# Optimization experiments

Hardware: AMD Instinct MI355X
Metric: run time of the kernel (lower is better)

Reference implementation:

```python
import jax, jax.numpy as jnp
import numpy as np
from math import sqrt

H = 16
D_MODEL = 1024
D_K = D_MODEL // H
B, S = 2, 2048


def setup_inputs() -> dict:
    key = jax.random.key(0)
    ks = jax.random.split(key, 12)
    scale = 1.0 / sqrt(D_MODEL)
    inp = {
        "query": jax.random.normal(ks[0], (B, S, D_MODEL), jnp.float32),
        "key": jax.random.normal(ks[1], (B, S, D_MODEL), jnp.float32),
        "value": jax.random.normal(ks[2], (B, S, D_MODEL), jnp.float32),
        # causal mask [B, S, S]; module unsqueezes head dim itself
        "mask": jnp.broadcast_to(jnp.tril(jnp.ones((S, S), jnp.int32)), (B, S, S)),
        "Wq": jax.random.normal(ks[3], (D_MODEL, D_MODEL), jnp.float32) * scale,
        "bq": jnp.zeros((D_MODEL,), jnp.float32),
        "Wk": jax.random.normal(ks[4], (D_MODEL, D_MODEL), jnp.float32) * scale,
        "bk": jnp.zeros((D_MODEL,), jnp.float32),
        "Wv": jax.random.normal(ks[5], (D_MODEL, D_MODEL), jnp.float32) * scale,
        "bv": jnp.zeros((D_MODEL,), jnp.float32),
        "Wo": jax.random.normal(ks[6], (D_MODEL, D_MODEL), jnp.float32) * scale,
        "bo": jnp.zeros((D_MODEL,), jnp.float32),
    }
    return inp


def reference(query, key, value, mask, Wq, bq, Wk, bk, Wv, bv, Wo, bo):
    nb = query.shape[0]

    def proj(x, W, b):
        # nn.Linear: x @ W.T + b, then split heads -> [B, H, S, D_K]
        y = jnp.einsum('bsd,ed->bse', x, W) + b
        return y.reshape(nb, -1, H, D_K).transpose(0, 2, 1, 3)

    q = proj(query, Wq, bq)
    k = proj(key, Wk, bk)
    v = proj(value, Wv, bv)

    scores = jnp.einsum('bhqd,bhkd->bhqk', q, k) / sqrt(D_K)  # [B,H,S,S]
    scores = jnp.where(mask[:, None, :, :] == 0, -jnp.inf, scores)
    probs = jax.nn.softmax(scores, axis=-1)  # dropout in eval mode (identity)
    ctx = jnp.einsum('bhqk,bhkd->bhqd', probs, v)
    ctx = ctx.transpose(0, 2, 1, 3).reshape(nb, -1, H * D_K)
    return jnp.einsum('bsd,ed->bse', ctx, Wo) + bo
```

## Files before the change

kernel.cpp:

```cpp
#include <hip/hip_runtime.h>
#include <hip/hip_bf16.h>
#include <stdint.h>


#define H_ 16
#define DM 1024
#define DK_ 64
#define BB 2
#define SS 2048
#define PSTR 72

typedef __bf16 bf16x8 __attribute__((ext_vector_type(8)));
typedef __bf16 bf16x2_t __attribute__((ext_vector_type(2)));
typedef float f32x4 __attribute__((ext_vector_type(4)));

#define GLOAD_LDS16(g, l)                                            \
  __builtin_amdgcn_global_load_lds(                                  \
      (__attribute__((address_space(1))) void*)(g),                  \
      (__attribute__((address_space(3))) void*)(l), 16, 0, 0)

__device__ __forceinline__ unsigned short f2bf_u(float f) {
  unsigned int u = __float_as_uint(f);
  u += 0x7fffu + ((u >> 16) & 1u);
  return (unsigned short)(u >> 16);
}

__device__ __forceinline__ unsigned int pack_bf16(float a, float b) {
#if __has_builtin(__builtin_amdgcn_cvt_pk_bf16_f32)
  bf16x2_t v = __builtin_amdgcn_cvt_pk_bf16_f32(a, b);
  unsigned int u;
  __builtin_memcpy(&u, &v, 4);
  return u;
#else
  return (unsigned int)f2bf_u(a) | ((unsigned int)f2bf_u(b) << 16);
#endif
}

__device__ __forceinline__ float fexp2(float x) {
#if __has_builtin(__builtin_amdgcn_exp2f)
  return __builtin_amdgcn_exp2f(x);
#else
  return exp2f(x);
#endif
}

struct Cvt {
  const float* s[7];
  unsigned short* d[7];
  int n[7];
};

__global__ __launch_bounds__(256) void convert_kernel(Cvt c) {
  const int y = blockIdx.y;
  const float* __restrict__ src = c.s[y];
  unsigned short* __restrict__ dst = c.d[y];
  const int nv = c.n[y] >> 2;
  for (int i = blockIdx.x * 256 + threadIdx.x; i < nv; i += 1024 * 256) {
    float4 v = *(const float4*)(src + (size_t)i * 4);
    ushort4 o;
    o.x = f2bf_u(v.x); o.y = f2bf_u(v.y); o.z = f2bf_u(v.z); o.w = f2bf_u(v.w);
    *(ushort4*)(dst + (size_t)i * 4) = o;
  }
}

template <int DUMMY = 0>
__device__ __forceinline__ void gemm_core(
    const unsigned short* __restrict__ A, const unsigned short* __restrict__ W,
    unsigned short* As, unsigned short* Bs, int m0, int n0, int k0, int k1,
    f32x4 (*acc)[4]) {
  const int tid = threadIdx.x;
  const int wave = tid >> 6, lane = tid & 63;
  const int lm = lane & 15, quad = lane >> 4;
  const int wm = (wave >> 1) * 64, wn = (wave & 1) * 64;
  const int srow = lane >> 2;
  const int scol = (lane & 3) * 8;

#pragma unroll
  for (int i = 0; i < 4; ++i)
#pragma unroll
    for (int j = 0; j < 4; ++j) {
      f32x4 z = {0.f, 0.f, 0.f, 0.f};
      acc[i][j] = z;
    }

  for (int kt = k0; kt < k1; kt += 32) {
#pragma unroll
    for (int cc = 0; cc < 2; ++cc) {
      int c = wave * 2 + cc;
      GLOAD_LDS16(A + (size_t)(m0 + c * 16 + srow) * DM + kt + scol,
                  As + c * 512 + lane * 8);
      GLOAD_LDS16(W + (size_t)(n0 + c * 16 + srow) * DM + kt + scol,
                  Bs + c * 512 + lane * 8);
    }
    __syncthreads();
    bf16x8 af[4], bfr[4];
#pragma unroll
    for (int i = 0; i < 4; ++i)
      af[i] = *(const bf16x8*)(As + (wm + i * 16 + lm) * 32 + quad * 8);
#pragma unroll
    for (int j = 0; j < 4; ++j)
      bfr[j] = *(const bf16x8*)(Bs + (wn + j * 16 + lm) * 32 + quad * 8);
#pragma unroll
    for (int i = 0; i < 4; ++i)
#pragma unroll
      for (int j = 0; j < 4; ++j)
        acc[i][j] = __builtin_amdgcn_mfma_f32_16x16x32_bf16(af[i], bfr[j],
                                                            acc[i][j], 0, 0, 0);
    __syncthreads();
  }
}

__global__ __launch_bounds__(256) void qkv_gemm(
    const unsigned short* Qi, const unsigned short* Ki, const unsigned short* Vi,
    const unsigned short* Wq, const unsigned short* Wk, const unsigned short* Wv,
    const float* bq, const float* bk, const float* bv,
    unsigned short* Qf, unsigned short* Kf, unsigned short* Vf) {
  __shared__ unsigned short As[128 * 32], Bs[128 * 32];
  const int z = blockIdx.z;
  const unsigned short* A = z == 0 ? Qi : (z == 1 ? Ki : Vi);
  const unsigned short* W = z == 0 ? Wq : (z == 1 ? Wk : Wv);
  const float* bias = z == 0 ? bq : (z == 1 ? bk : bv);
  const float scale = z == 0 ? 0.125f : 1.0f;
  const int m0 = blockIdx.y * 128, n0 = blockIdx.x * 128;
  f32x4 acc[4][4];
  gemm_core(A, W, As, Bs, m0, n0, 0, DM, acc);
  const int lane = threadIdx.x & 63, wave = threadIdx.x >> 6;
  const int lm = lane & 15, quad = lane >> 4;
  const int wm = (wave >> 1) * 64, wn = (wave & 1) * 64;
  if (z == 2) {
#pragma unroll
    for (int j = 0; j < 4; ++j) {
      int gn = n0 + wn + j * 16 + lm;
      float bv_ = bias[gn];
      int h2 = gn >> 6, dk = gn & 63;
      int a = dk >> 4, ln = dk & 15;
#pragma unroll
      for (int i = 0; i < 4; ++i) {
        int s0 = m0 + wm + i * 16 + quad * 4;
        int b2 = s0 >> 11, sl = s0 & 2047;
        int kt2 = sl >> 6, cc = (sl >> 5) & 1, qk = (sl >> 3) & 3, j0 = sl & 7;
        size_t base =
            ((size_t)(((b2 * 16 + h2) * 32 + kt2) * 4 + a) * 2 + cc) * 512 +
            (qk * 16 + ln) * 8 + j0;
        uint2 w;
        w.x = pack_bf16(acc[i][j][0] + bv_, acc[i][j][1] + bv_);
        w.y = pack_bf16(acc[i][j][2] + bv_, acc[i][j][3] + bv_);
        *(uint2*)(Vf + base) = w;
      }
    }
  } else {
    unsigned short* out = z == 0 ? Qf : Kf;
#pragma unroll
    for (int j = 0; j < 4; ++j) {
      int gn = n0 + wn + j * 16 + lm;
      float bv_ = bias[gn];
      int h2 = gn >> 6, d64 = gn & 63;
      int cc = (d64 >> 5) & 1, qk = (d64 >> 3) & 3, jj = d64 & 7;
#pragma unroll
      for (int i = 0; i < 4; ++i)
#pragma unroll
        for (int r = 0; r < 4; ++r) {
          int gm = m0 + wm + i * 16 + quad * 4 + r;
          int b2 = gm >> 11, sl = gm & 2047;
          size_t base =
              ((size_t)((b2 * 16 + h2) * 128 + (sl >> 4)) * 2 + cc) * 512 +
              (qk * 16 + (sl & 15)) * 8 + jj;
          out[base] = f2bf_u((acc[i][j][r] + bv_) * scale);
        }
    }
  }
}

__global__ __launch_bounds__(256) void o_gemm_sk(
    const unsigned short* Ctx, const unsigned short* Wo,
    float* P0, float* P1) {
  __shared__ unsigned short As[128 * 32], Bs[128 * 32];
  const int m0 = blockIdx.y * 128, n0 = blockIdx.x * 128, ks = blockIdx.z;
  f32x4 acc[4][4];
  gemm_core(Ctx, Wo, As, Bs, m0, n0, ks * 512, ks * 512 + 512, acc);
  const int lane = threadIdx.x & 63, wave = threadIdx.x >> 6;
  const int lm = lane & 15, quad = lane >> 4;
  const int wm = (wave >> 1) * 64, wn = (wave & 1) * 64;
  float* dst = ks ? P1 : P0;
#pragma unroll
  for (int j = 0; j < 4; ++j) {
    int gn = n0 + wn + j * 16 + lm;
#pragma unroll
    for (int i = 0; i < 4; ++i)
#pragma unroll
      for (int r = 0; r < 4; ++r) {
        int gm = m0 + wm + i * 16 + quad * 4 + r;
        dst[(size_t)gm * DM + gn] = acc[i][j][r];
      }
  }
}

__global__ __launch_bounds__(256) void o_reduce(
    const float4* __restrict__ P0, const float4* __restrict__ P1,
    const float* __restrict__ bo, float4* __restrict__ out) {
  for (int i = blockIdx.x * 256 + threadIdx.x; i < 1048576; i += 1024 * 256) {
    float4 a = P0[i], b = P1[i];
    float4 bb = *(const float4*)(bo + (i & 255) * 4);
    float4 o;
    o.x = a.x + b.x + bb.x; o.y = a.y + b.y + bb.y;
    o.z = a.z + b.z + bb.z; o.w = a.w + b.w + bb.w;
    out[i] = o;
  }
}

__global__ __launch_bounds__(256, 4) void attn_kernel(
    const unsigned short* __restrict__ Qf, const unsigned short* __restrict__ Kf,
    const unsigned short* __restrict__ Vf, unsigned short* __restrict__ Ctx) {
  __shared__ unsigned short Ps[4][16 * PSTR];
  const int p = blockIdx.x;
  const int bh = p & 31, qb0 = p >> 5;
  const int qb = (bh & 1) ? (31 - qb0) : qb0;
  const int b = bh >> 4, h = bh & 15;
  const int tid = threadIdx.x, wave = tid >> 6, lane = tid & 63;
  const int lm = lane & 15, quad = lane >> 4;
  const float L2E = 1.4426950408889634f;

  const int qbase = qb * 64 + wave * 16;
  const int nkw = qb + 1;

  bf16x8 qf[2];
#pragma unroll
  for (int c = 0; c < 2; ++c)
    qf[c] = *(const bf16x8*)(Qf +
        ((size_t)(bh * 128 + (qbase >> 4)) * 2 + c) * 512 + lane * 8);

  const unsigned short* Kb = Kf + (size_t)bh * 256 * 512;
  const unsigned short* Vb = Vf + (size_t)bh * 256 * 512;
  unsigned short* Pw = Ps[wave];

  float lsum = 0.f;
  f32x4 oacc[4];
#pragma unroll
  for (int a = 0; a < 4; ++a) {
    f32x4 z = {0.f, 0.f, 0.f, 0.f};
    oacc[a] = z;
  }

  for (int kt = 0; kt < nkw; ++kt) {
    bf16x8 kf[4][2];
#pragma unroll
    for (int ik = 0; ik < 4; ++ik)
#pragma unroll
      for (int c = 0; c < 2; ++c)
        kf[ik][c] = *(const bf16x8*)(Kb +
            ((size_t)(kt * 4 + ik) * 2 + c) * 512 + lane * 8);
    f32x4 s[4];
#pragma unroll
    for (int ik = 0; ik < 4; ++ik) {
      f32x4 z = {0.f, 0.f, 0.f, 0.f};
      z = __builtin_amdgcn_mfma_f32_16x16x32_bf16(kf[ik][0], qf[0], z, 0, 0, 0);
      s[ik] = __builtin_amdgcn_mfma_f32_16x16x32_bf16(kf[ik][1], qf[1], z, 0, 0, 0);
    }
    if (kt == nkw - 1) {
#pragma unroll
      for (int ik = 0; ik < 4; ++ik)
#pragma unroll
        for (int r = 0; r < 4; ++r) {
          int kg = kt * 64 + ik * 16 + quad * 4 + r;
          int qg = qbase + lm;
          if (kg > qg) s[ik][r] = -1e30f;
        }
    }

    bf16x8 vf[4][2];
#pragma unroll
    for (int a = 0; a < 4; ++a)
#pragma unroll
      for (int c = 0; c < 2; ++c)
        vf[a][c] = *(const bf16x8*)(Vb +
            ((size_t)(kt * 8 + a * 2 + c)) * 512 + lane * 8);

#pragma unroll
    for (int ik = 0; ik < 4; ++ik) {
      float p0 = fexp2(s[ik][0] * L2E);
      float p1 = fexp2(s[ik][1] * L2E);
      float p2 = fexp2(s[ik][2] * L2E);
      float p3 = fexp2(s[ik][3] * L2E);
      lsum += (p0 + p1) + (p2 + p3);
      uint2 w;
      w.x = pack_bf16(p0, p1);
      w.y = pack_bf16(p2, p3);
      *(uint2*)(Pw + lm * PSTR + ik * 16 + quad * 4) = w;
    }

    bf16x8 pf[2];
#pragma unroll
    for (int c = 0; c < 2; ++c)
      pf[c] = *(const bf16x8*)(Pw + lm * PSTR + c * 32 + quad * 8);
#pragma unroll
    for (int a = 0; a < 4; ++a) {
      oacc[a] = __builtin_amdgcn_mfma_f32_16x16x32_bf16(pf[0], vf[a][0], oacc[a], 0, 0, 0);
      oacc[a] = __builtin_amdgcn_mfma_f32_16x16x32_bf16(pf[1], vf[a][1], oacc[a], 0, 0, 0);
    }
  }

  lsum += __shfl_xor(lsum, 16);
  lsum += __shfl_xor(lsum, 32);
#pragma unroll
  for (int r = 0; r < 4; ++r) {
    float inv = 1.0f / __shfl(lsum, quad * 4 + r);
    int qg = qbase + quad * 4 + r;
#pragma unroll
    for (int a = 0; a < 4; ++a)
      Ctx[(size_t)(b * SS + qg) * DM + h * DK_ + a * 16 + lm] =
          f2bf_u(oacc[a][r] * inv);
  }
}

extern "C" void kernel_launch(void* const* d_in, const int* in_sizes, int n_in,
                              void* d_out, int out_size, void* d_ws, size_t ws_size,
                              hipStream_t stream) {
  const float* q = (const float*)d_in[0];
  const float* k = (const float*)d_in[1];
  const float* v = (const float*)d_in[2];
  const float* Wq = (const float*)d_in[4];
  const float* bq = (const float*)d_in[5];
  const float* Wk = (const float*)d_in[6];
  const float* bk = (const float*)d_in[7];
  const float* Wv = (const float*)d_in[8];
  const float* bv = (const float*)d_in[9];
  const float* Wo = (const float*)d_in[10];
  const float* bo = (const float*)d_in[11];

  const size_t NX = (size_t)BB * SS * DM;
  const size_t NW = (size_t)DM * DM;
  unsigned short* ws = (unsigned short*)d_ws;
  unsigned short* Qi = ws;
  unsigned short* Ki = Qi + NX;
  unsigned short* Vi = Ki + NX;
  unsigned short* Wqb = Vi + NX;
  unsigned short* Wkb = Wqb + NW;
  unsigned short* Wvb = Wkb + NW;
  unsigned short* Wob = Wvb + NW;
  unsigned short* Qfr = Wob + NW;
  unsigned short* Kfr = Qfr + NX;
  unsigned short* Vfr = Kfr + NX;
  unsigned short* Ctx = Vfr + NX;
  float* P0 = (float*)ws;
  float* P1 = (float*)Qfr;

  Cvt c;
  c.s[0] = q; c.s[1] = k; c.s[2] = v; c.s[3] = Wq; c.s[4] = Wk; c.s[5] = Wv; c.s[6] = Wo;
  c.d[0] = Qi; c.d[1] = Ki; c.d[2] = Vi; c.d[3] = Wqb; c.d[4] = Wkb; c.d[5] = Wvb; c.d[6] = Wob;
  c.n[0] = c.n[1] = c.n[2] = (int)NX;
  c.n[3] = c.n[4] = c.n[5] = c.n[6] = (int)NW;

  dim3 blk(256);
  convert_kernel<<<dim3(1024, 7), blk, 0, stream>>>(c);
  qkv_gemm<<<dim3(8, 32, 3), blk, 0, stream>>>(Qi, Ki, Vi, Wqb, Wkb, Wvb,
                                               bq, bk, bv, Qfr, Kfr, Vfr);
  attn_kernel<<<dim3(1024), blk, 0, stream>>>(Qfr, Kfr, Vfr, Ctx);
  o_gemm_sk<<<dim3(8, 32, 2), blk, 0, stream>>>(Ctx, Wob, P0, P1);
  o_reduce<<<dim3(1024), blk, 0, stream>>>((const float4*)P0, (const float4*)P1,
                                           bo, (float4*)d_out);
}
```

Before: 263.3 us.

## Fuse fp32-to-bf16 activation conversion into QKV GEMM A-tile loads and swizzle block order

Stops converting the query, key and value activations to bf16 in a separate pass. The QKV GEMM now reads fp32 activations directly, packs them to bf16 in registers and stores them to LDS, so only the weights still go through the conversion kernel. This removes a full write and re-read of three activation tensors. The QKV and output-projection GEMMs also move to a 1D grid with a remapped block order that groups M tiles per chunk, likely for L2 reuse. The cost is that A loads in the QKV GEMM become synchronous register loads instead of async global-to-LDS copies, and they fetch twice the bytes per element.

Result: slower. 292.4 us (+11.1%).

```diff
diff --git a/kernel.cpp b/kernel.cpp
--- a/kernel.cpp
+++ b/kernel.cpp
@@ -45,17 +45,15 @@
 }
 
 struct Cvt {
-  const float* s[7];
-  unsigned short* d[7];
-  int n[7];
+  const float* s[4];
+  unsigned short* d[4];
 };
 
 __global__ __launch_bounds__(256) void convert_kernel(Cvt c) {
   const int y = blockIdx.y;
   const float* __restrict__ src = c.s[y];
   unsigned short* __restrict__ dst = c.d[y];
-  const int nv = c.n[y] >> 2;
-  for (int i = blockIdx.x * 256 + threadIdx.x; i < nv; i += 1024 * 256) {
+  for (int i = blockIdx.x * 256 + threadIdx.x; i < (1 << 18); i += 256 * 256) {
     float4 v = *(const float4*)(src + (size_t)i * 4);
     ushort4 o;
     o.x = f2bf_u(v.x); o.y = f2bf_u(v.y); o.z = f2bf_u(v.z); o.w = f2bf_u(v.w);
@@ -110,20 +108,80 @@
   }
 }
 
+template <int DUMMY = 0>
+__device__ __forceinline__ void gemm_core_f32A(
+    const float* __restrict__ A, const unsigned short* __restrict__ W,
+    unsigned short* As, unsigned short* Bs, int m0, int n0,
+    f32x4 (*acc)[4]) {
+  const int tid = threadIdx.x;
+  const int wave = tid >> 6, lane = tid & 63;
+  const int lm = lane & 15, quad = lane >> 4;
+  const int wm = (wave >> 1) * 64, wn = (wave & 1) * 64;
+  const int srow = lane >> 2;
+  const int scol = (lane & 3) * 8;
+  const int arow = tid >> 1, acol = (tid & 1) * 16;
+
+#pragma unroll
+  for (int i = 0; i < 4; ++i)
+#pragma unroll
+    for (int j = 0; j < 4; ++j) {
+      f32x4 z = {0.f, 0.f, 0.f, 0.f};
+      acc[i][j] = z;
+    }
+
+  for (int kt = 0; kt < DM; kt += 32) {
+#pragma unroll
+    for (int cc = 0; cc < 2; ++cc) {
+      int c = wave * 2 + cc;
+      GLOAD_LDS16(W + (size_t)(n0 + c * 16 + srow) * DM + kt + scol,
+                  Bs + c * 512 + lane * 8);
+    }
+    const float* ga = A + (size_t)(m0 + arow) * DM + kt + acol;
+    float4 f0 = *(const float4*)(ga);
+    float4 f1 = *(const float4*)(ga + 4);
+    float4 f2 = *(const float4*)(ga + 8);
+    float4 f3 = *(const float4*)(ga + 12);
+    uint4 u0 = {pack_bf16(f0.x, f0.y), pack_bf16(f0.z, f0.w),
+                pack_bf16(f1.x, f1.y), pack_bf16(f1.z, f1.w)};
+    uint4 u1 = {pack_bf16(f2.x, f2.y), pack_bf16(f2.z, f2.w),
+                pack_bf16(f3.x, f3.y), pack_bf16(f3.z, f3.w)};
+    *(uint4*)(As + arow * 32 + acol) = u0;
+    *(uint4*)(As + arow * 32 + acol + 8) = u1;
+    __syncthreads();
+    bf16x8 af[4], bfr[4];
+#pragma unroll
+    for (int i = 0; i < 4; ++i)
+      af[i] = *(const bf16x8*)(As + (wm + i * 16 + lm) * 32 + quad * 8);
+#pragma unroll
+    for (int j = 0; j < 4; ++j)
+      bfr[j] = *(const bf16x8*)(Bs + (wn + j * 16 + lm) * 32 + quad * 8);
+#pragma unroll
+    for (int i = 0; i < 4; ++i)
+#pragma unroll
+      for (int j = 0; j < 4; ++j)
+        acc[i][j] = __builtin_amdgcn_mfma_f32_16x16x32_bf16(af[i], bfr[j],
+                                                            acc[i][j], 0, 0, 0);
+    __syncthreads();
+  }
+}
+
 __global__ __launch_bounds__(256) void qkv_gemm(
-    const unsigned short* Qi, const unsigned short* Ki, const unsigned short* Vi,
+    const float* q32, const float* k32, const float* v32,
     const unsigned short* Wq, const unsigned short* Wk, const unsigned short* Wv,
     const float* bq, const float* bk, const float* bv,
     unsigned short* Qf, unsigned short* Kf, unsigned short* Vf) {
   __shared__ unsigned short As[128 * 32], Bs[128 * 32];
-  const int z = blockIdx.z;
-  const unsigned short* A = z == 0 ? Qi : (z == 1 ? Ki : Vi);
+  const int p = blockIdx.x;
+  const int c = p & 7, jj0 = p >> 3;
+  const int x = jj0 & 7, yy = (jj0 >> 3) & 3, z = jj0 >> 5;
+  const int y = c * 4 + yy;
+  const int m0 = y * 128, n0 = x * 128;
+  const float* A = z == 0 ? q32 : (z == 1 ? k32 : v32);
   const unsigned short* W = z == 0 ? Wq : (z == 1 ? Wk : Wv);
   const float* bias = z == 0 ? bq : (z == 1 ? bk : bv);
   const float scale = z == 0 ? 0.125f : 1.0f;
-  const int m0 = blockIdx.y * 128, n0 = blockIdx.x * 128;
   f32x4 acc[4][4];
-  gemm_core(A, W, As, Bs, m0, n0, 0, DM, acc);
+  gemm_core_f32A(A, W, As, Bs, m0, n0, acc);
   const int lane = threadIdx.x & 63, wave = threadIdx.x >> 6;
   const int lm = lane & 15, quad = lane >> 4;
   const int wm = (wave >> 1) * 64, wn = (wave & 1) * 64;
@@ -155,7 +213,7 @@
       int gn = n0 + wn + j * 16 + lm;
       float bv_ = bias[gn];
       int h2 = gn >> 6, d64 = gn & 63;
-      int cc = (d64 >> 5) & 1, qk = (d64 >> 3) & 3, jj = d64 & 7;
+      int cc = (d64 >> 5) & 1, qk = (d64 >> 3) & 3, jjq = d64 & 7;
 #pragma unroll
       for (int i = 0; i < 4; ++i)
 #pragma unroll
@@ -164,7 +222,7 @@
           int b2 = gm >> 11, sl = gm & 2047;
           size_t base =
               ((size_t)((b2 * 16 + h2) * 128 + (sl >> 4)) * 2 + cc) * 512 +
-              (qk * 16 + (sl & 15)) * 8 + jj;
+              (qk * 16 + (sl & 15)) * 8 + jjq;
           out[base] = f2bf_u((acc[i][j][r] + bv_) * scale);
         }
     }
@@ -175,7 +233,11 @@
     const unsigned short* Ctx, const unsigned short* Wo,
     float* P0, float* P1) {
   __shared__ unsigned short As[128 * 32], Bs[128 * 32];
-  const int m0 = blockIdx.y * 128, n0 = blockIdx.x * 128, ks = blockIdx.z;
+  const int p = blockIdx.x;
+  const int c = p & 7, jj0 = p >> 3;
+  const int x = jj0 & 7, yy = (jj0 >> 3) & 3, ks = jj0 >> 5;
+  const int y = c * 4 + yy;
+  const int m0 = y * 128, n0 = x * 128;
   f32x4 acc[4][4];
   gemm_core(Ctx, Wo, As, Bs, m0, n0, ks * 512, ks * 512 + 512, acc);
   const int lane = threadIdx.x & 63, wave = threadIdx.x >> 6;
@@ -330,10 +392,7 @@
   const size_t NX = (size_t)BB * SS * DM;
   const size_t NW = (size_t)DM * DM;
   unsigned short* ws = (unsigned short*)d_ws;
-  unsigned short* Qi = ws;
-  unsigned short* Ki = Qi + NX;
-  unsigned short* Vi = Ki + NX;
-  unsigned short* Wqb = Vi + NX;
+  unsigned short* Wqb = ws;
   unsigned short* Wkb = Wqb + NW;
   unsigned short* Wvb = Wkb + NW;
   unsigned short* Wob = Wvb + NW;
@@ -341,21 +400,19 @@
   unsigned short* Kfr = Qfr + NX;
   unsigned short* Vfr = Kfr + NX;
   unsigned short* Ctx = Vfr + NX;
-  float* P0 = (float*)ws;
-  float* P1 = (float*)Qfr;
+  float* P0 = (float*)Qfr;
+  float* P1 = (float*)(Ctx + NX);
 
   Cvt c;
-  c.s[0] = q; c.s[1] = k; c.s[2] = v; c.s[3] = Wq; c.s[4] = Wk; c.s[5] = Wv; c.s[6] = Wo;
-  c.d[0] = Qi; c.d[1] = Ki; c.d[2] = Vi; c.d[3] = Wqb; c.d[4] = Wkb; c.d[5] = Wvb; c.d[6] = Wob;
-  c.n[0] = c.n[1] = c.n[2] = (int)NX;
-  c.n[3] = c.n[4] = c.n[5] = c.n[6] = (int)NW;
+  c.s[0] = Wq; c.s[1] = Wk; c.s[2] = Wv; c.s[3] = Wo;
+  c.d[0] = Wqb; c.d[1] = Wkb; c.d[2] = Wvb; c.d[3] = Wob;
 
   dim3 blk(256);
-  convert_kernel<<<dim3(1024, 7), blk, 0, stream>>>(c);
-  qkv_gemm<<<dim3(8, 32, 3), blk, 0, stream>>>(Qi, Ki, Vi, Wqb, Wkb, Wvb,
-                                               bq, bk, bv, Qfr, Kfr, Vfr);
+  convert_kernel<<<dim3(256, 4), blk, 0, stream>>>(c);
+  qkv_gemm<<<dim3(768), blk, 0, stream>>>(q, k, v, Wqb, Wkb, Wvb,
+                                          bq, bk, bv, Qfr, Kfr, Vfr);
   attn_kernel<<<dim3(1024), blk, 0, stream>>>(Qfr, Kfr, Vfr, Ctx);
-  o_gemm_sk<<<dim3(8, 32, 2), blk, 0, stream>>>(Ctx, Wob, P0, P1);
+  o_gemm_sk<<<dim3(512), blk, 0, stream>>>(Ctx, Wob, P0, P1);
   o_reduce<<<dim3(1024), blk, 0, stream>>>((const float4*)P0, (const float4*)P1,
                                            bo, (float4*)d_out);
 }
```
